# Optimization experiments

Hardware: AMD Instinct MI355X
Metric: run time of the kernel (lower is better)

Reference implementation:

```python
import jax, jax.numpy as jnp
import numpy as np

BS, SEQ, FT_IN = 64, 576, 768
HID, HEADS, FT_OUT = 512, 4, 512
N = SEQ + 1  # pooled node + tokens
NUM_NODES = BS * N


def _build_edges():
    # star graph per sample: 0 <-> (1+j) both directions, then self loops, batched with offsets
    j = np.arange(SEQ)
    src = np.empty(2 * SEQ, np.int32); dst = np.empty(2 * SEQ, np.int32)
    src[0::2] = 0;      dst[0::2] = 1 + j
    src[1::2] = 1 + j;  dst[1::2] = 0
    loops = np.arange(N, dtype=np.int32)
    src = np.concatenate([src, loops]); dst = np.concatenate([dst, loops])
    offs = (np.arange(BS, dtype=np.int32) * N)[:, None]
    return (src[None, :] + offs).reshape(-1), (dst[None, :] + offs).reshape(-1)


def setup_inputs() -> dict:
    key = jax.random.key(0)
    ks = jax.random.split(key, 24)
    s = 0.02
    src, dst = _build_edges()
    return {
        "hidden_states": jax.random.normal(ks[0], (BS, SEQ, FT_IN), jnp.float32),
        "pooled_output": jax.random.normal(ks[1], (BS, HID), jnp.float32),
        # SeqLinear projector: 768 -> 512 -> 512
        "pw1": jax.random.normal(ks[2], (FT_IN, HID)) * s, "pb1": jnp.zeros((HID,)),
        "pw2": jax.random.normal(ks[3], (HID, HID)) * s, "pb2": jnp.zeros((HID,)),
        # GATv2 conv1: 512 -> 4 heads x 128
        "wl1": jax.random.normal(ks[4], (HID, HID)) * s, "bl1": jnp.zeros((HID,)),
        "wr1": jax.random.normal(ks[5], (HID, HID)) * s, "br1": jnp.zeros((HID,)),
        "att1": jax.random.normal(ks[6], (HEADS, HID // HEADS)) * s,
        "bias1": jnp.zeros((HID,)),
        # GATv2 conv2: 512 -> 1 head x 512
        "wl2": jax.random.normal(ks[7], (HID, HID)) * s, "bl2": jnp.zeros((HID,)),
        "wr2": jax.random.normal(ks[8], (HID, HID)) * s, "br2": jnp.zeros((HID,)),
        "att2": jax.random.normal(ks[9], (1, HID)) * s,
        "bias2": jnp.zeros((HID,)),
        # final lin: 512 -> 512
        "linw": jax.random.normal(ks[10], (HID, FT_OUT)) * s, "linb": jnp.zeros((FT_OUT,)),
        "src": jnp.asarray(src), "dst": jnp.asarray(dst),
    }


def _gatv2(x, src, dst, wl, bl, wr, br, att, bias, heads, cout, num_nodes):
    # PyG GATv2Conv (share_weights=False), eval mode (attn dropout off)
    xl = (x @ wl + bl).reshape(num_nodes, heads, cout)  # source transform (messages)
    xr = (x @ wr + br).reshape(num_nodes, heads, cout)  # target transform
    z = jax.nn.leaky_relu(xl[src] + xr[dst], negative_slope=0.2)  # [E,H,C]
    e = jnp.einsum('ehc,hc->eh', z, att)                          # [E,H]
    m = jax.ops.segment_max(e, dst, num_segments=num_nodes)
    p = jnp.exp(e - m[dst])
    s = jax.ops.segment_sum(p, dst, num_segments=num_nodes)
    alpha = p / (s[dst] + 1e-16)                                  # segment softmax over in-edges
    out = jax.ops.segment_sum(xl[src] * alpha[..., None], dst, num_segments=num_nodes)
    return out.reshape(num_nodes, heads * cout) + bias


def reference(hidden_states, pooled_output, pw1, pb1, pw2, pb2,
              wl1, bl1, wr1, br1, att1, bias1,
              wl2, bl2, wr2, br2, att2, bias2,
              linw, linb, src, dst):
    bs, seq, _ = hidden_states.shape
    n = seq + 1
    num_nodes = bs * n
    # ProjLayers / SeqLinear (eval: dropout identity); GELU between layers
    h = jax.nn.gelu(hidden_states @ pw1 + pb1)
    h = h @ pw2 + pb2                                    # [bs, seq, 512]
    x = jnp.concatenate([pooled_output[:, None, :], h], axis=1)  # [bs, n, 512]
    x = x.reshape(num_nodes, -1)
    # GNN: GATv2 -> GELU -> GATv2
    h1 = jax.nn.gelu(_gatv2(x, src, dst, wl1, bl1, wr1, br1, att1, bias1, HEADS, HID // HEADS, num_nodes))
    h2 = _gatv2(h1, src, dst, wl2, bl2, wr2, br2, att2, bias2, 1, HID, num_nodes)
    h2b = h2.reshape(bs, n, -1)
    graph_mean = h2b.mean(axis=1)                        # global_mean_pool (contiguous graphs)
    cls = h2b[:, 0, :]                                   # node 0 per graph; dropout off (eval)
    out = cls @ linw + linb + pooled_output
    return out, graph_mean
```

## Files before the change

### kernel.cpp

```cpp
#include <hip/hip_runtime.h>
#include <hip/hip_bf16.h>
#include <math.h>

constexpr int BSZ       = 64;
constexpr int SEQL      = 576;
constexpr int FTIN      = 768;
constexpr int HID       = 512;
constexpr int NNODE     = SEQL + 1;
constexpr int NUM_NODES = BSZ * NNODE;
constexpr int MROWS     = BSZ * SEQL;

using b8 = __attribute__((ext_vector_type(8))) __bf16;
using f4 = __attribute__((ext_vector_type(4))) float;
typedef unsigned short u16;

__device__ __forceinline__ float gelu_f(float x) {
    float x3 = x * x * x;
    return 0.5f * x * (1.0f + tanhf(0.7978845608028654f * (x + 0.044715f * x3)));
}
__device__ __forceinline__ float lrelu(float x) {
    return x > 0.0f ? x : 0.2f * x;
}
__device__ __forceinline__ u16 f2bf(float v) {
    __hip_bfloat16 b = __float2bfloat16(v);
    return __builtin_bit_cast(u16, b);
}
__device__ __forceinline__ float bf2f(u16 u) {
    return __bfloat162float(__builtin_bit_cast(__hip_bfloat16, u));
}
__device__ __forceinline__ void split_bf(float v, u16& h, u16& l) {
    h = f2bf(v);
    l = f2bf(v - bf2f(h));
}
__device__ __forceinline__ void gl16(const void* g, void* l) {
    __builtin_amdgcn_global_load_lds(
        (const __attribute__((address_space(1))) unsigned int*)g,
        (__attribute__((address_space(3))) unsigned int*)l, 16, 0, 0);
}
__device__ __forceinline__ f4 mfma16(b8 a, b8 b, f4 c) {
    return __builtin_amdgcn_mfma_f32_16x16x32_bf16(a, b, c, 0, 0, 0);
}

__global__ __launch_bounds__(256) void transpose_split_k(
    const float* __restrict__ W, u16* __restrict__ Th,
    u16* __restrict__ Tl, int K, int N)
{
    __shared__ float t[64][65];
    const int kb = blockIdx.x * 64, nb = blockIdx.y * 64;
    for (int i = threadIdx.x; i < 64 * 64; i += 256) {
        int r = i >> 6, c = i & 63;
        t[r][c] = W[(size_t)(kb + r) * N + nb + c];
    }
    __syncthreads();
    for (int i = threadIdx.x; i < 64 * 64; i += 256) {
        int r = i >> 6, c = i & 63;
        float v = t[c][r];
        u16 h, l; split_bf(v, h, l);
        Th[(size_t)(nb + r) * K + kb + c] = h;
        Tl[(size_t)(nb + r) * K + kb + c] = l;
    }
}

__global__ __launch_bounds__(256) void fuse_bias_k(
    const float* __restrict__ pb,
    const float* __restrict__ wA, const float* __restrict__ wB,
    const float* __restrict__ bA, const float* __restrict__ bB,
    float* __restrict__ out)
{
    const int n = blockIdx.x * 256 + threadIdx.x;
    const float* W = (n < 512) ? wA : wB;
    const int c = n & 511;
    float acc = 0.0f;
    if (pb) {
        for (int j = 0; j < 512; j++) acc = fmaf(pb[j], W[(size_t)j * 512 + c], acc);
    }
    out[n] = acc + ((n < 512) ? bA[c] : bB[c]);
}

__global__ __launch_bounds__(256) void node0_proj_k(
    const float* __restrict__ pooled,
    const float* __restrict__ wl, const float* __restrict__ wr,
    const float* __restrict__ bl, const float* __restrict__ br,
    float* __restrict__ XL, float* __restrict__ XR)
{
    const int b = blockIdx.x;
    const int n = blockIdx.y * 256 + threadIdx.x;
    __shared__ float p[HID];
    for (int k = threadIdx.x; k < HID; k += 256) p[k] = pooled[b * HID + k];
    __syncthreads();
    const float* W = (n < 512) ? wl : wr;
    const int c = n & 511;
    float acc = 0.0f;
    for (int k = 0; k < HID; k++) acc = fmaf(p[k], W[(size_t)k * 512 + c], acc);
    acc += (n < 512) ? bl[c] : br[c];
    const size_t row = (size_t)b * NNODE * HID;
    if (n < 512) XL[row + c] = acc; else XR[row + c] = acc;
}

template<int MODE, bool AF32>
__global__ __launch_bounds__(256, 2) void bgemm(
    const u16* __restrict__ Ah, const u16* __restrict__ Al,
    const float* __restrict__ Af,
    const u16* __restrict__ BTh, const u16* __restrict__ BTl,
    const float* __restrict__ bias,
    float* __restrict__ CfL, float* __restrict__ CfR,
    u16* __restrict__ Ch, u16* __restrict__ Cl,
    int M, int K)
{
    __shared__ u16 lds[2][4][4096];

    const int tid  = threadIdx.x;
    const int wid  = tid >> 6, lane = tid & 63;
    const int wr   = wid >> 1, wc = wid & 1;
    const int lrow = lane & 15, lk = lane >> 4;
    const int row0 = blockIdx.x * 128, col0 = blockIdx.y * 128;
    const int nt   = K >> 5;

    f4 acc[4][4] = {};
    float4 areg[4];

    auto STAGE = [&](int buf, int k0) {
#pragma unroll
        for (int i = 0; i < 2; i++) {
            const int r = wid * 2 + i;
            const int bcol = col0 + r * 16 + lrow;
            const size_t bgo = (size_t)bcol * K + k0 + lk * 8;
            gl16(BTh + bgo, &lds[buf][2][r * 512]);
            gl16(BTl + bgo, &lds[buf][3][r * 512]);
            if constexpr (!AF32) {
                int grow = row0 + r * 16 + lrow;
                if (grow >= M) grow = M - 1;
                const size_t ago = (size_t)grow * K + k0 + lk * 8;
                gl16(Ah + ago, &lds[buf][0][r * 512]);
                gl16(Al + ago, &lds[buf][1][r * 512]);
            }
        }
    };
    auto ALOAD = [&](int k0) {
#pragma unroll
        for (int q = 0; q < 4; q++) {
            const int ch = tid * 4 + q;
            const int r = ch >> 3, c4 = ch & 7;
            areg[q] = *(const float4*)(Af + (size_t)(row0 + r) * K + k0 + c4 * 4);
        }
    };
    auto AWRITE = [&](int buf) {
#pragma unroll
        for (int q = 0; q < 4; q++) {
            const int ch = tid * 4 + q;
            const int r = ch >> 3, c4 = ch & 7;
            u16 h0, l0, h1, l1, h2, l2, h3, l3;
            split_bf(areg[q].x, h0, l0); split_bf(areg[q].y, h1, l1);
            split_bf(areg[q].z, h2, l2); split_bf(areg[q].w, h3, l3);
            const int off = (r >> 4) * 512 + ((c4 >> 1) * 16 + (r & 15)) * 8 + (c4 & 1) * 4;
            *(ushort4*)&lds[buf][0][off] = make_ushort4(h0, h1, h2, h3);
            *(ushort4*)&lds[buf][1][off] = make_ushort4(l0, l1, l2, l3);
        }
    };

    if constexpr (AF32) { ALOAD(0); AWRITE(0); }
    STAGE(0, 0);
    __syncthreads();

    for (int t = 0; t < nt; t++) {
        const int cur = t & 1;
        const bool more = (t + 1 < nt);
        if (more) {
            if constexpr (AF32) ALOAD((t + 1) << 5);
            STAGE(cur ^ 1, (t + 1) << 5);
        }
        b8 a_h[4], b_h[4], tmp[4];
#pragma unroll
        for (int m = 0; m < 4; m++) a_h[m] = *(const b8*)&lds[cur][0][(wr * 4 + m) * 512 + lane * 8];
#pragma unroll
        for (int n = 0; n < 4; n++) b_h[n] = *(const b8*)&lds[cur][2][(wc * 4 + n) * 512 + lane * 8];
#pragma unroll
        for (int m = 0; m < 4; m++)
#pragma unroll
            for (int n = 0; n < 4; n++)
                acc[m][n] = mfma16(a_h[m], b_h[n], acc[m][n]);
#pragma unroll
        for (int m = 0; m < 4; m++) tmp[m] = *(const b8*)&lds[cur][1][(wr * 4 + m) * 512 + lane * 8];
#pragma unroll
        for (int m = 0; m < 4; m++)
#pragma unroll
            for (int n = 0; n < 4; n++)
                acc[m][n] = mfma16(tmp[m], b_h[n], acc[m][n]);
#pragma unroll
        for (int n = 0; n < 4; n++) tmp[n] = *(const b8*)&lds[cur][3][(wc * 4 + n) * 512 + lane * 8];
#pragma unroll
        for (int m = 0; m < 4; m++)
#pragma unroll
            for (int n = 0; n < 4; n++)
                acc[m][n] = mfma16(a_h[m], tmp[n], acc[m][n]);

        if constexpr (AF32) { if (more) AWRITE(cur ^ 1); }
        __syncthreads();
    }

    const int gcolbase = col0 + wc * 64;
    float biasn[4];
    if constexpr (MODE != 3) {
#pragma unroll
        for (int n = 0; n < 4; n++) biasn[n] = bias[gcolbase + n * 16 + lrow];
    }

#pragma unroll
    for (int m = 0; m < 4; m++) {
#pragma unroll
        for (int r = 0; r < 4; r++) {
            const int grow = row0 + wr * 64 + m * 16 + lk * 4 + r;
            if (MODE != 5 || grow < M) {
#pragma unroll
                for (int n = 0; n < 4; n++) {
                    const int gcol = gcolbase + n * 16 + lrow;
                    float v = acc[m][n][r];
                    if constexpr (MODE == 1) {
                        v = gelu_f(v + biasn[n]);
                        u16 h, l; split_bf(v, h, l);
                        Ch[(size_t)grow * HID + gcol] = h;
                        Cl[(size_t)grow * HID + gcol] = l;
                    } else if constexpr (MODE == 3) {
                        u16 h, l; split_bf(v, h, l);
                        Ch[(size_t)gcol * 512 + grow] = h;
                        Cl[(size_t)gcol * 512 + grow] = l;
                    } else {
                        v += biasn[n];
                        const int orow = (MODE == 4) ? (grow + grow / SEQL + 1) : grow;
                        if (gcol < 512) CfL[(size_t)orow * HID + gcol] = v;
                        else            CfR[(size_t)orow * HID + gcol - 512] = v;
                    }
                }
            }
        }
    }
}

template<int HEADS, bool GELU, bool OSPLIT>
__global__ __launch_bounds__(256) void gat_edge_k(
    const float* __restrict__ xl, const float* __restrict__ xr,
    const float* __restrict__ att, const float* __restrict__ bias,
    float* __restrict__ outF, u16* __restrict__ outH, u16* __restrict__ outL)
{
    const int b = blockIdx.x / SEQL;
    const int j = blockIdx.x % SEQL;
    const size_t row0 = (size_t)(b * NNODE) * HID;
    const size_t rowj = (size_t)(b * NNODE + 1 + j) * HID;
    const int t = threadIdx.x;
    const int c = 2 * t;

    const float2 xl0  = *(const float2*)(xl + row0 + c);
    const float2 xljv = *(const float2*)(xl + rowj + c);
    const float2 xrjv = *(const float2*)(xr + rowj + c);
    const float2 attc = *(const float2*)(att + c);

    float e0 = attc.x * lrelu(xl0.x + xrjv.x) + attc.y * lrelu(xl0.y + xrjv.y);
    float e1 = attc.x * lrelu(xljv.x + xrjv.x) + attc.y * lrelu(xljv.y + xrjv.y);

#pragma unroll
    for (int off = 32; off; off >>= 1) {
        e0 += __shfl_down(e0, off, 64);
        e1 += __shfl_down(e1, off, 64);
    }
    __shared__ float s0[4], s1[4];
    const int w = t >> 6, lane = t & 63;
    if (lane == 0) { s0[w] = e0; s1[w] = e1; }
    __syncthreads();

    float E0, E1;
    if (HEADS == 4) { E0 = s0[w]; E1 = s1[w]; }
    else            { E0 = s0[0] + s0[1] + s0[2] + s0[3];
                      E1 = s1[0] + s1[1] + s1[2] + s1[3]; }

    const float m  = fmaxf(E0, E1);
    const float p0 = expf(E0 - m);
    const float p1 = expf(E1 - m);
    const float inv = 1.0f / (p0 + p1 + 1e-16f);
    const float a0 = p0 * inv, a1 = p1 * inv;

    float ox = a0 * xl0.x + a1 * xljv.x + bias[c + 0];
    float oy = a0 * xl0.y + a1 * xljv.y + bias[c + 1];
    if (GELU) { ox = gelu_f(ox); oy = gelu_f(oy); }
    if constexpr (OSPLIT) {
        u16 h0, l0, h1, l1;
        split_bf(ox, h0, l0); split_bf(oy, h1, l1);
        *(ushort2*)&outH[rowj + c] = make_ushort2(h0, h1);
        *(ushort2*)&outL[rowj + c] = make_ushort2(l0, l1);
    } else {
        *(float2*)(outF + rowj + c) = make_float2(ox, oy);
    }
}

template<int HEADS, bool GELU, bool OSPLIT>
__global__ __launch_bounds__(256) void gat_node0_k(
    const float* __restrict__ xl, const float* __restrict__ xr,
    const float* __restrict__ att, const float* __restrict__ bias,
    float* __restrict__ outF, u16* __restrict__ outH, u16* __restrict__ outL)
{
    constexpr int CH = HID / HEADS;
    const int b = blockIdx.x;
    const int h = blockIdx.y;
    const int t = threadIdx.x;
    const size_t base = (size_t)(b * NNODE) * HID;

    __shared__ float xr0s[CH];
    __shared__ float es[NNODE];
    __shared__ float red[256];

    const float* atth = att + h * CH;
    for (int c = t; c < CH; c += 256) xr0s[c] = xr[base + h * CH + c];
    __syncthreads();

    for (int s = t; s < NNODE; s += 256) {
        const float* xls = xl + base + (size_t)s * HID + h * CH;
        float e = 0.0f;
        for (int c = 0; c < CH; c += 4) {
            float4 v = *(const float4*)(xls + c);
            float4 a = *(const float4*)(atth + c);
            e = fmaf(a.x, lrelu(v.x + xr0s[c + 0]), e);
            e = fmaf(a.y, lrelu(v.y + xr0s[c + 1]), e);
            e = fmaf(a.z, lrelu(v.z + xr0s[c + 2]), e);
            e = fmaf(a.w, lrelu(v.w + xr0s[c + 3]), e);
        }
        es[s] = e;
    }
    __syncthreads();

    float m = -INFINITY;
    for (int s = t; s < NNODE; s += 256) m = fmaxf(m, es[s]);
    red[t] = m; __syncthreads();
    for (int off = 128; off; off >>= 1) {
        if (t < off) red[t] = fmaxf(red[t], red[t + off]);
        __syncthreads();
    }
    m = red[0];
    __syncthreads();

    float sum = 0.0f;
    for (int s = t; s < NNODE; s += 256) {
        float p = expf(es[s] - m);
        es[s] = p;
        sum += p;
    }
    red[t] = sum; __syncthreads();
    for (int off = 128; off; off >>= 1) {
        if (t < off) red[t] += red[t + off];
        __syncthreads();
    }
    const float invS = 1.0f / (red[0] + 1e-16f);

    for (int c = t; c < CH; c += 256) {
        float acc = 0.0f;
        for (int s = 0; s < NNODE; s++)
            acc = fmaf(es[s], xl[base + (size_t)s * HID + h * CH + c], acc);
        float o = acc * invS + bias[h * CH + c];
        if (GELU) o = gelu_f(o);
        if constexpr (OSPLIT) {
            u16 hh, ll; split_bf(o, hh, ll);
            outH[base + h * CH + c] = hh;
            outL[base + h * CH + c] = ll;
        } else {
            outF[base + h * CH + c] = o;
        }
    }
}

__global__ __launch_bounds__(256) void mean_k(const float* __restrict__ h2,
                                              float* __restrict__ out)
{
    const int b = blockIdx.x;
    const int c = blockIdx.y * 256 + threadIdx.x;
    const float* p = h2 + (size_t)(b * NNODE) * HID + c;
    float s = 0.0f;
    for (int i = 0; i < NNODE; i++) s += p[(size_t)i * HID];
    out[(size_t)BSZ * HID + b * HID + c] = s * (1.0f / NNODE);
}

__global__ __launch_bounds__(256) void head_k(
    const float* __restrict__ h2, const float* __restrict__ linw,
    const float* __restrict__ linb, const float* __restrict__ pooled,
    float* __restrict__ out)
{
    const int b = blockIdx.x;
    const int col = blockIdx.y * 256 + threadIdx.x;
    __shared__ float cls[HID];
    for (int k = threadIdx.x; k < HID; k += 256)
        cls[k] = h2[(size_t)(b * NNODE) * HID + k];
    __syncthreads();
    float acc = 0.0f;
    for (int k = 0; k < HID; k++)
        acc = fmaf(cls[k], linw[(size_t)k * HID + col], acc);
    out[b * HID + col] = acc + linb[col] + pooled[b * HID + col];
}

extern "C" void kernel_launch(void* const* d_in, const int* in_sizes, int n_in,
                              void* d_out, int out_size, void* d_ws, size_t ws_size,
                              hipStream_t stream)
{
    const float* hs     = (const float*)d_in[0];
    const float* pooled = (const float*)d_in[1];
    const float* pw1  = (const float*)d_in[2];  const float* pb1   = (const float*)d_in[3];
    const float* pw2  = (const float*)d_in[4];  const float* pb2   = (const float*)d_in[5];
    const float* wl1  = (const float*)d_in[6];  const float* bl1   = (const float*)d_in[7];
    const float* wr1  = (const float*)d_in[8];  const float* br1   = (const float*)d_in[9];
    const float* att1 = (const float*)d_in[10]; const float* bias1 = (const float*)d_in[11];
    const float* wl2  = (const float*)d_in[12]; const float* bl2   = (const float*)d_in[13];
    const float* wr2  = (const float*)d_in[14]; const float* br2   = (const float*)d_in[15];
    const float* att2 = (const float*)d_in[16]; const float* bias2 = (const float*)d_in[17];
    const float* linw = (const float*)d_in[18]; const float* linb  = (const float*)d_in[19];
    float* out = (float*)d_out;

    char* ws = (char*)d_ws;
    const size_t RSZ = 75637760;
    char* R0 = ws;
    char* R1 = ws + RSZ;
    char* R2 = ws + 2 * RSZ;
    u16*  Wr = (u16*)(ws + 3 * RSZ);

    u16* hH  = (u16*)R0;
    u16* hL  = hH + (size_t)MROWS * HID;
    u16* h1H = (u16*)R0;
    u16* h1L = h1H + (size_t)NUM_NODES * HID;
    float* h2 = (float*)R0;
    float* XL = (float*)R1;
    float* XR = (float*)R2;
    u16* prepBT_h = (u16*)R1;
    u16* prepBT_l = prepBT_h + 1024 * 512;
    u16* pw1T_h   = prepBT_l + 1024 * 512;
    u16* pw1T_l   = pw1T_h + 512 * FTIN;
    u16* W1Th = Wr;
    u16* W1Tl = W1Th + 1024 * 512;
    u16* BT2h = W1Tl + 1024 * 512;
    u16* BT2l = BT2h + 1024 * 512;
    float* fb1 = (float*)(BT2l + 1024 * 512);
    float* fb2 = fb1 + 1024;

    const dim3 blk(256);

    transpose_split_k<<<dim3(8, 8), blk, 0, stream>>>(wl1, prepBT_h, prepBT_l, HID, HID);
    transpose_split_k<<<dim3(8, 8), blk, 0, stream>>>(wr1, prepBT_h + 512 * 512, prepBT_l + 512 * 512, HID, HID);
    transpose_split_k<<<dim3(12, 8), blk, 0, stream>>>(pw1, pw1T_h, pw1T_l, FTIN, HID);
    transpose_split_k<<<dim3(8, 8), blk, 0, stream>>>(wl2, BT2h, BT2l, HID, HID);
    transpose_split_k<<<dim3(8, 8), blk, 0, stream>>>(wr2, BT2h + 512 * 512, BT2l + 512 * 512, HID, HID);
    bgemm<3, true><<<dim3(4, 8), blk, 0, stream>>>(nullptr, nullptr, pw2, prepBT_h, prepBT_l,
                                                   nullptr, nullptr, nullptr, W1Th, W1Tl, 512, HID);
    fuse_bias_k<<<dim3(4), blk, 0, stream>>>(pb2, wl1, wr1, bl1, br1, fb1);
    fuse_bias_k<<<dim3(4), blk, 0, stream>>>(nullptr, wl2, wr2, bl2, br2, fb2);

    bgemm<1, true><<<dim3(288, 4), blk, 0, stream>>>(nullptr, nullptr, hs, pw1T_h, pw1T_l,
                                                     pb1, nullptr, nullptr, hH, hL, MROWS, FTIN);
    bgemm<4, false><<<dim3(288, 8), blk, 0, stream>>>(hH, hL, nullptr, W1Th, W1Tl,
                                                      fb1, XL, XR, nullptr, nullptr, MROWS, HID);
    node0_proj_k<<<dim3(BSZ, 4), blk, 0, stream>>>(pooled, wl1, wr1, bl1, br1, XL, XR);
    gat_edge_k<4, true, true><<<dim3(MROWS), blk, 0, stream>>>(XL, XR, att1, bias1,
                                                               nullptr, h1H, h1L);
    gat_node0_k<4, true, true><<<dim3(BSZ, 4), blk, 0, stream>>>(XL, XR, att1, bias1,
                                                                 nullptr, h1H, h1L);
    bgemm<5, false><<<dim3(289, 8), blk, 0, stream>>>(h1H, h1L, nullptr, BT2h, BT2l,
                                                      fb2, XL, XR, nullptr, nullptr, NUM_NODES, HID);
    gat_edge_k<1, false, false><<<dim3(MROWS), blk, 0, stream>>>(XL, XR, att2, bias2,
                                                                 h2, nullptr, nullptr);
    gat_node0_k<1, false, false><<<dim3(BSZ, 1), blk, 0, stream>>>(XL, XR, att2, bias2,
                                                                   h2, nullptr, nullptr);
    head_k<<<dim3(BSZ, 2), blk, 0, stream>>>(h2, linw, linb, pooled, out);
    mean_k<<<dim3(BSZ, 2), blk, 0, stream>>>(h2, out);
}
```

Before: 1.164 ms.

## Single-buffer bgemm LDS, raise occupancy, remap blocks via 1D XCD-aware swizzle

The bgemm kernel drops its double-buffered LDS pipeline in favour of a single buffer that is loaded and then synchronised each k-step. This halves LDS use and lets launch bounds ask for 4 blocks per CU instead of 2. The 2D grid becomes a 1D grid whose block index is remapped so that consecutive tiles land on the same XCD (8-way interleave), aimed at better L2 reuse. The cost is that global-load latency is no longer overlapped with MFMA work inside a block, and the design relies on the extra resident blocks to hide it.

Result: faster. 1.078 ms (-7.4%).

```diff
diff --git a/kernel.cpp b/kernel.cpp
--- a/kernel.cpp
+++ b/kernel.cpp
@@ -98,103 +98,95 @@
 }
 
 template<int MODE, bool AF32>
-__global__ __launch_bounds__(256, 2) void bgemm(
+__global__ __launch_bounds__(256, 4) void bgemm(
     const u16* __restrict__ Ah, const u16* __restrict__ Al,
     const float* __restrict__ Af,
     const u16* __restrict__ BTh, const u16* __restrict__ BTl,
     const float* __restrict__ bias,
     float* __restrict__ CfL, float* __restrict__ CfR,
     u16* __restrict__ Ch, u16* __restrict__ Cl,
-    int M, int K)
-{
-    __shared__ u16 lds[2][4][4096];
+    int M, int K, int nblk)
+{
+    __shared__ u16 lds[4][4096];
+
+    const int nwg = gridDim.x;
+    const int p = blockIdx.x;
+    const int lb = (nwg % 8 == 0) ? (p % 8) * (nwg / 8) + p / 8 : p;
+    const int row0 = (lb / nblk) * 128, col0 = (lb % nblk) * 128;
 
     const int tid  = threadIdx.x;
     const int wid  = tid >> 6, lane = tid & 63;
     const int wr   = wid >> 1, wc = wid & 1;
     const int lrow = lane & 15, lk = lane >> 4;
-    const int row0 = blockIdx.x * 128, col0 = blockIdx.y * 128;
     const int nt   = K >> 5;
 
     f4 acc[4][4] = {};
     float4 areg[4];
 
-    auto STAGE = [&](int buf, int k0) {
+    for (int t = 0; t < nt; t++) {
+        const int k0 = t << 5;
+
 #pragma unroll
         for (int i = 0; i < 2; i++) {
             const int r = wid * 2 + i;
             const int bcol = col0 + r * 16 + lrow;
             const size_t bgo = (size_t)bcol * K + k0 + lk * 8;
-            gl16(BTh + bgo, &lds[buf][2][r * 512]);
-            gl16(BTl + bgo, &lds[buf][3][r * 512]);
+            gl16(BTh + bgo, &lds[2][r * 512]);
+            gl16(BTl + bgo, &lds[3][r * 512]);
             if constexpr (!AF32) {
                 int grow = row0 + r * 16 + lrow;
                 if (grow >= M) grow = M - 1;
                 const size_t ago = (size_t)grow * K + k0 + lk * 8;
-                gl16(Ah + ago, &lds[buf][0][r * 512]);
-                gl16(Al + ago, &lds[buf][1][r * 512]);
+                gl16(Ah + ago, &lds[0][r * 512]);
+                gl16(Al + ago, &lds[1][r * 512]);
             }
         }
-    };
-    auto ALOAD = [&](int k0) {
-#pragma unroll
-        for (int q = 0; q < 4; q++) {
-            const int ch = tid * 4 + q;
-            const int r = ch >> 3, c4 = ch & 7;
-            areg[q] = *(const float4*)(Af + (size_t)(row0 + r) * K + k0 + c4 * 4);
+        if constexpr (AF32) {
+#pragma unroll
+            for (int q = 0; q < 4; q++) {
+                const int ch = tid * 4 + q;
+                const int r = ch >> 3, c4 = ch & 7;
+                areg[q] = *(const float4*)(Af + (size_t)(row0 + r) * K + k0 + c4 * 4);
+            }
+#pragma unroll
+            for (int q = 0; q < 4; q++) {
+                const int ch = tid * 4 + q;
+                const int r = ch >> 3, c4 = ch & 7;
+                u16 h0, l0, h1, l1, h2, l2, h3, l3;
+                split_bf(areg[q].x, h0, l0); split_bf(areg[q].y, h1, l1);
+                split_bf(areg[q].z, h2, l2); split_bf(areg[q].w, h3, l3);
+                const int off = (r >> 4) * 512 + ((c4 >> 1) * 16 + (r & 15)) * 8 + (c4 & 1) * 4;
+                *(ushort4*)&lds[0][off] = make_ushort4(h0, h1, h2, h3);
+                *(ushort4*)&lds[1][off] = make_ushort4(l0, l1, l2, l3);
+            }
         }
-    };
-    auto AWRITE = [&](int buf) {
-#pragma unroll
-        for (int q = 0; q < 4; q++) {
-            const int ch = tid * 4 + q;
-            const int r = ch >> 3, c4 = ch & 7;
-            u16 h0, l0, h1, l1, h2, l2, h3, l3;
-            split_bf(areg[q].x, h0, l0); split_bf(areg[q].y, h1, l1);
-            split_bf(areg[q].z, h2, l2); split_bf(areg[q].w, h3, l3);
-            const int off = (r >> 4) * 512 + ((c4 >> 1) * 16 + (r & 15)) * 8 + (c4 & 1) * 4;
-            *(ushort4*)&lds[buf][0][off] = make_ushort4(h0, h1, h2, h3);
-            *(ushort4*)&lds[buf][1][off] = make_ushort4(l0, l1, l2, l3);
-        }
-    };
-
-    if constexpr (AF32) { ALOAD(0); AWRITE(0); }
-    STAGE(0, 0);
-    __syncthreads();
-
-    for (int t = 0; t < nt; t++) {
-        const int cur = t & 1;
-        const bool more = (t + 1 < nt);
-        if (more) {
-            if constexpr (AF32) ALOAD((t + 1) << 5);
-            STAGE(cur ^ 1, (t + 1) << 5);
-        }
+        __syncthreads();
+
         b8 a_h[4], b_h[4], tmp[4];
 #pragma unroll
-        for (int m = 0; m < 4; m++) a_h[m] = *(const b8*)&lds[cur][0][(wr * 4 + m) * 512 + lane * 8];
-#pragma unroll
-        for (int n = 0; n < 4; n++) b_h[n] = *(const b8*)&lds[cur][2][(wc * 4 + n) * 512 + lane * 8];
+        for (int m = 0; m < 4; m++) a_h[m] = *(const b8*)&lds[0][(wr * 4 + m) * 512 + lane * 8];
+#pragma unroll
+        for (int n = 0; n < 4; n++) b_h[n] = *(const b8*)&lds[2][(wc * 4 + n) * 512 + lane * 8];
 #pragma unroll
         for (int m = 0; m < 4; m++)
 #pragma unroll
             for (int n = 0; n < 4; n++)
                 acc[m][n] = mfma16(a_h[m], b_h[n], acc[m][n]);
 #pragma unroll
-        for (int m = 0; m < 4; m++) tmp[m] = *(const b8*)&lds[cur][1][(wr * 4 + m) * 512 + lane * 8];
+        for (int m = 0; m < 4; m++) tmp[m] = *(const b8*)&lds[1][(wr * 4 + m) * 512 + lane * 8];
 #pragma unroll
         for (int m = 0; m < 4; m++)
 #pragma unroll
             for (int n = 0; n < 4; n++)
                 acc[m][n] = mfma16(tmp[m], b_h[n], acc[m][n]);
 #pragma unroll
-        for (int n = 0; n < 4; n++) tmp[n] = *(const b8*)&lds[cur][3][(wc * 4 + n) * 512 + lane * 8];
+        for (int n = 0; n < 4; n++) tmp[n] = *(const b8*)&lds[3][(wc * 4 + n) * 512 + lane * 8];
 #pragma unroll
         for (int m = 0; m < 4; m++)
 #pragma unroll
             for (int n = 0; n < 4; n++)
                 acc[m][n] = mfma16(a_h[m], tmp[n], acc[m][n]);
 
-        if constexpr (AF32) { if (more) AWRITE(cur ^ 1); }
         __syncthreads();
     }
 
@@ -442,22 +434,22 @@
     transpose_split_k<<<dim3(12, 8), blk, 0, stream>>>(pw1, pw1T_h, pw1T_l, FTIN, HID);
     transpose_split_k<<<dim3(8, 8), blk, 0, stream>>>(wl2, BT2h, BT2l, HID, HID);
     transpose_split_k<<<dim3(8, 8), blk, 0, stream>>>(wr2, BT2h + 512 * 512, BT2l + 512 * 512, HID, HID);
-    bgemm<3, true><<<dim3(4, 8), blk, 0, stream>>>(nullptr, nullptr, pw2, prepBT_h, prepBT_l,
-                                                   nullptr, nullptr, nullptr, W1Th, W1Tl, 512, HID);
+    bgemm<3, true><<<dim3(32), blk, 0, stream>>>(nullptr, nullptr, pw2, prepBT_h, prepBT_l,
+                                                 nullptr, nullptr, nullptr, W1Th, W1Tl, 512, HID, 8);
     fuse_bias_k<<<dim3(4), blk, 0, stream>>>(pb2, wl1, wr1, bl1, br1, fb1);
     fuse_bias_k<<<dim3(4), blk, 0, stream>>>(nullptr, wl2, wr2, bl2, br2, fb2);
 
-    bgemm<1, true><<<dim3(288, 4), blk, 0, stream>>>(nullptr, nullptr, hs, pw1T_h, pw1T_l,
-                                                     pb1, nullptr, nullptr, hH, hL, MROWS, FTIN);
-    bgemm<4, false><<<dim3(288, 8), blk, 0, stream>>>(hH, hL, nullptr, W1Th, W1Tl,
-                                                      fb1, XL, XR, nullptr, nullptr, MROWS, HID);
+    bgemm<1, true><<<dim3(1152), blk, 0, stream>>>(nullptr, nullptr, hs, pw1T_h, pw1T_l,
+                                                   pb1, nullptr, nullptr, hH, hL, MROWS, FTIN, 4);
+    bgemm<4, false><<<dim3(2304), blk, 0, stream>>>(hH, hL, nullptr, W1Th, W1Tl,
+                                                    fb1, XL, XR, nullptr, nullptr, MROWS, HID, 8);
     node0_proj_k<<<dim3(BSZ, 4), blk, 0, stream>>>(pooled, wl1, wr1, bl1, br1, XL, XR);
     gat_edge_k<4, true, true><<<dim3(MROWS), blk, 0, stream>>>(XL, XR, att1, bias1,
                                                                nullptr, h1H, h1L);
     gat_node0_k<4, true, true><<<dim3(BSZ, 4), blk, 0, stream>>>(XL, XR, att1, bias1,
                                                                  nullptr, h1H, h1L);
-    bgemm<5, false><<<dim3(289, 8), blk, 0, stream>>>(h1H, h1L, nullptr, BT2h, BT2l,
-                                                      fb2, XL, XR, nullptr, nullptr, NUM_NODES, HID);
+    bgemm<5, false><<<dim3(2312), blk, 0, stream>>>(h1H, h1L, nullptr, BT2h, BT2l,
+                                                    fb2, XL, XR, nullptr, nullptr, NUM_NODES, HID, 8);
     gat_edge_k<1, false, false><<<dim3(MROWS), blk, 0, stream>>>(XL, XR, att2, bias2,
                                                                  h2, nullptr, nullptr);
     gat_node0_k<1, false, false><<<dim3(BSZ, 1), blk, 0, stream>>>(XL, XR, att2, bias2,
```
